# Optimization experiments

Measured on AMD Instinct MI355X. Metric: run time of the kernel, lower is better.

## Reference

```python
import jax, jax.numpy as jnp
import numpy as np

T, B, DIM, N, K = 512, 32, 1024, 256, 32  # K = checkpoint interval, divides T


def setup_inputs() -> dict:
    key = jax.random.key(0)
    k1, k2, k3, k4 = jax.random.split(key, 4)
    scale = 1.0 / np.sqrt(DIM)  # keep projections O(1) like trained weights
    return {
        "x": jax.random.normal(k1, (T, B, DIM), dtype=jnp.float32),
        "S0": jnp.zeros((B, N, N), dtype=jnp.float32),
        "W_k": jax.random.normal(k2, (N, DIM), dtype=jnp.float32) * scale,
        "W_v": jax.random.normal(k3, (N, DIM), dtype=jnp.float32) * scale,
        "W_q": jax.random.normal(k4, (N, DIM), dtype=jnp.float32) * scale,
    }


def reference(x, S0, W_k, W_v, W_q):
    # Projections (batched GEMMs), done once up-front as in the torch code.
    k_all = jnp.einsum("tbd,nd->tbn", x, W_k)
    v_all = jnp.einsum("tbd,nd->tbn", x, W_v)
    q_all = jnp.einsum("tbd,nd->tbn", x, W_q)
    k_norm = k_all / (jnp.linalg.norm(k_all, axis=-1, keepdims=True) + 1e-6)

    def step(S, kvq):
        kn, v, q = kvq  # each [B, N]
        retrieved = jnp.einsum("bij,bj->bi", S, kn)          # S @ k_norm
        S = S + (v - retrieved)[:, :, None] * kn[:, None, :]  # rank-1 delta write
        Sq = jnp.einsum("bij,bj->bi", S, q)                   # readout with updated S
        out = Sq * jax.nn.silu(Sq)
        return S, out

    def segment(S, kvq_seg):
        return jax.lax.scan(step, S, kvq_seg)

    nseg = T // K
    seg_kvq = (
        k_norm.reshape(nseg, K, B, N),
        v_all.reshape(nseg, K, B, N),
        q_all.reshape(nseg, K, B, N),
    )
    _, outs = jax.lax.scan(segment, S0, seg_kvq)  # [nseg, K, B, N]
    return outs.reshape(T, B, N)
```

## Files before the change

### kernel.cpp

```cpp
#include <hip/hip_runtime.h>
#include <hip/hip_bf16.h>
#include <math.h>

#define T_DIM 512
#define B_DIM 32
#define D_DIM 1024
#define N_DIM 256
#define M_DIM (T_DIM * B_DIM)
#define CHUNK 32
#define NCHUNK (T_DIM / CHUNK)
#define IBLK 32
#define ST (B_DIM * N_DIM)
#define BK 32

typedef _Float16 f16;
typedef _Float16 f16x8 __attribute__((ext_vector_type(8)));
typedef _Float16 f16x4 __attribute__((ext_vector_type(4)));
typedef __fp16   h16x2 __attribute__((ext_vector_type(2)));
typedef float    f32x4 __attribute__((ext_vector_type(4)));

#define LDK 264
#define LDT 40
#define LDV 36

#define GLOAD_LDS16(g, l)                                         \
  __builtin_amdgcn_global_load_lds(                               \
      (const __attribute__((address_space(1))) void*)(g),         \
      (__attribute__((address_space(3))) void*)(l), 16, 0, 0)

__device__ __forceinline__ f16x8 cvt8(const float4& a, const float4& b) {
  f16x8 h;
  h[0] = (f16)a.x; h[1] = (f16)a.y; h[2] = (f16)a.z; h[3] = (f16)a.w;
  h[4] = (f16)b.x; h[5] = (f16)b.y; h[6] = (f16)b.z; h[7] = (f16)b.w;
  return h;
}

__device__ __forceinline__ f16x8 pk8(const f32x4 a, const f32x4 b) {
  union { f16x8 v; h16x2 p[4]; } u;
  u.p[0] = __builtin_amdgcn_cvt_pkrtz(a[0], a[1]);
  u.p[1] = __builtin_amdgcn_cvt_pkrtz(a[2], a[3]);
  u.p[2] = __builtin_amdgcn_cvt_pkrtz(b[0], b[1]);
  u.p[3] = __builtin_amdgcn_cvt_pkrtz(b[2], b[3]);
  return u.v;
}

__global__ __launch_bounds__(256) void cvt_w_kernel(
    const float* __restrict__ wk, const float* __restrict__ wv,
    const float* __restrict__ wq, f16* __restrict__ out) {
  const int i = (blockIdx.x * 256 + threadIdx.x) * 8;
  const int m = blockIdx.y;
  const float* src = (m == 0) ? wk : (m == 1) ? wv : wq;
  const float4 f0 = *(const float4*)(src + i);
  const float4 f1 = *(const float4*)(src + i + 4);
  *(f16x8*)(out + (size_t)m * (N_DIM * D_DIM) + i) = cvt8(f0, f1);
}

__global__ __launch_bounds__(256, 3) void proj_gemm_mfma(
    const float* __restrict__ x, const f16* __restrict__ Wh,
    f16* __restrict__ ok, f16* __restrict__ ov, f16* __restrict__ oq) {
  __shared__ __align__(16) float Af[2][128 * BK];
  __shared__ __align__(16) f16   Bh[2][128 * BK];

  const int tid  = threadIdx.x;
  const int lane = tid & 63;
  const int w    = tid >> 6;
  const int wm   = w >> 1, wn = w & 1;
  const int lr   = lane & 15;
  const int lq   = lane >> 4;

  const int mb  = blockIdx.x * 128;
  const int mat = blockIdx.y >> 1;
  const int nb  = (blockIdx.y & 1) * 128;

  const f16* Wmat = Wh + (size_t)mat * (N_DIM * D_DIM) + (size_t)nb * D_DIM;
  f16*       C    = (mat == 0) ? ok : (mat == 1) ? ov : oq;

  const int ar  = lane >> 3;
  const int acq = (lane & 7) ^ ar;
  const int brr = lane >> 2;
  const int bco = lane & 3;

  f32x4 acc[4][4];
  #pragma unroll
  for (int i = 0; i < 4; ++i)
    #pragma unroll
    for (int j = 0; j < 4; ++j) acc[i][j] = (f32x4){0.f, 0.f, 0.f, 0.f};

  #pragma unroll
  for (int j = 0; j < 4; ++j) {
    const int r = 32 * j + 8 * w + ar;
    GLOAD_LDS16(x + (size_t)(mb + r) * D_DIM + acq * 4, &Af[0][(32 * j + 8 * w) * BK]);
  }
  #pragma unroll
  for (int j = 0; j < 2; ++j) {
    const int r = 64 * j + 16 * w + brr;
    GLOAD_LDS16(Wmat + (size_t)r * D_DIM + bco * 8, &Bh[0][(64 * j + 16 * w) * BK]);
  }
  __syncthreads();

  int cur = 0;
  for (int kt = 0; kt < D_DIM; kt += BK) {
    if (kt + BK < D_DIM) {
      #pragma unroll
      for (int j = 0; j < 4; ++j) {
        const int r = 32 * j + 8 * w + ar;
        GLOAD_LDS16(x + (size_t)(mb + r) * D_DIM + kt + BK + acq * 4,
                    &Af[cur ^ 1][(32 * j + 8 * w) * BK]);
      }
      #pragma unroll
      for (int j = 0; j < 2; ++j) {
        const int r = 64 * j + 16 * w + brr;
        GLOAD_LDS16(Wmat + (size_t)r * D_DIM + kt + BK + bco * 8,
                    &Bh[cur ^ 1][(64 * j + 16 * w) * BK]);
      }
    }
    {
      f16x8 af[4], bf[4];
      #pragma unroll
      for (int mi = 0; mi < 4; ++mi) {
        const int row = 64 * wm + 16 * mi + lr;
        const int q0  = (2 * lq)     ^ (row & 7);
        const int q1  = (2 * lq + 1) ^ (row & 7);
        const f32x4 a0 = *(const f32x4*)&Af[cur][row * BK + q0 * 4];
        const f32x4 a1 = *(const f32x4*)&Af[cur][row * BK + q1 * 4];
        af[mi] = pk8(a0, a1);
      }
      #pragma unroll
      for (int nj = 0; nj < 4; ++nj) {
        const int row = 64 * wn + 16 * nj + lr;
        bf[nj] = *(const f16x8*)&Bh[cur][row * BK + lq * 8];
      }
      #pragma unroll
      for (int mi = 0; mi < 4; ++mi)
        #pragma unroll
        for (int nj = 0; nj < 4; ++nj)
          acc[mi][nj] = __builtin_amdgcn_mfma_f32_16x16x32_f16(af[mi], bf[nj], acc[mi][nj], 0, 0, 0);
    }
    __syncthreads();
    cur ^= 1;
  }

  #pragma unroll
  for (int mi = 0; mi < 4; ++mi)
    #pragma unroll
    for (int nj = 0; nj < 4; ++nj)
      #pragma unroll
      for (int r = 0; r < 4; ++r) {
        const int rg = mb + 64 * wm + 16 * mi + 4 * lq + r;
        const int cg = nb + 64 * wn + 16 * nj + lr;
        C[(size_t)rg * N_DIM + cg] = (f16)acc[mi][nj][r];
      }
}

__global__ __launch_bounds__(256) void knorm_kernel(f16* __restrict__ k) {
  const int w    = threadIdx.x >> 6;
  const int lane = threadIdx.x & 63;
  const int row  = blockIdx.x * 4 + w;
  f16* p = k + (size_t)row * N_DIM + lane * 4;
  f16x4 h = *reinterpret_cast<const f16x4*>(p);
  const float x0 = (float)h[0], x1 = (float)h[1], x2 = (float)h[2], x3 = (float)h[3];
  float ss = x0 * x0 + x1 * x1 + x2 * x2 + x3 * x3;
  #pragma unroll
  for (int m = 1; m < 64; m <<= 1) ss += __shfl_xor(ss, m, 64);
  const float inv = 1.0f / (sqrtf(ss) + 1e-6f);
  h[0] = (f16)(x0 * inv); h[1] = (f16)(x1 * inv);
  h[2] = (f16)(x2 * inv); h[3] = (f16)(x3 * inv);
  *reinterpret_cast<f16x4*>(p) = h;
}

__global__ __launch_bounds__(256, 2) void precompute_wg(
    const f16* __restrict__ kn, const f16* __restrict__ q,
    f16* __restrict__ Wg, f16* __restrict__ Gg, f16* __restrict__ KTg) {
  __shared__ __align__(16) f16 Kh[32 * LDK];
  __shared__ __align__(16) f16 Qh[32 * LDK];
  __shared__ float Al[32 * 33];

  const int tid  = threadIdx.x;
  const int lane = tid & 63;
  const int w    = tid >> 6;
  const int lr   = lane & 15;
  const int lq   = lane >> 4;
  const int tm   = w >> 1, tn = w & 1;
  const int b    = blockIdx.x >> 4;
  const int c    = blockIdx.x & 15;
  const int t0g  = c * CHUNK;

  {
    const int t = tid >> 3, cg = tid & 7;
    const f16* ks = kn + (size_t)(t0g + t) * ST + b * N_DIM + cg * 32;
    const f16* qs = q  + (size_t)(t0g + t) * ST + b * N_DIM + cg * 32;
    #pragma unroll
    for (int m = 0; m < 4; ++m) {
      *(f16x8*)&Kh[t * LDK + cg * 32 + 8 * m] = ((const f16x8*)ks)[m];
      *(f16x8*)&Qh[t * LDK + cg * 32 + 8 * m] = ((const f16x8*)qs)[m];
    }
  }
  __syncthreads();

  {
    f16* kt_dst = KTg + ((size_t)blockIdx.x * N_DIM + tid) * CHUNK;
    #pragma unroll
    for (int t8 = 0; t8 < 4; ++t8) {
      f16x8 h;
      #pragma unroll
      for (int e = 0; e < 8; ++e) h[e] = Kh[(8 * t8 + e) * LDK + tid];
      *(f16x8*)(kt_dst + 8 * t8) = h;
    }
  }

  f32x4 Aa = {0.f, 0.f, 0.f, 0.f}, Ga = {0.f, 0.f, 0.f, 0.f};
  #pragma unroll
  for (int kk = 0; kk < 8; ++kk) {
    f16x8 ka = *(const f16x8*)&Kh[(16 * tm + lr) * LDK + 32 * kk + 8 * lq];
    f16x8 qa = *(const f16x8*)&Qh[(16 * tm + lr) * LDK + 32 * kk + 8 * lq];
    f16x8 kb = *(const f16x8*)&Kh[(16 * tn + lr) * LDK + 32 * kk + 8 * lq];
    Aa = __builtin_amdgcn_mfma_f32_16x16x32_f16(ka, kb, Aa, 0, 0, 0);
    Ga = __builtin_amdgcn_mfma_f32_16x16x32_f16(qa, kb, Ga, 0, 0, 0);
  }
  {
    const int s = 16 * tn + lr;
    f16* gdst = Gg + (size_t)blockIdx.x * 1280;
    #pragma unroll
    for (int r = 0; r < 4; ++r) {
      const int t = 16 * tm + 4 * lq + r;
      Al[t * 33 + s] = (s < t) ? Aa[r] : 0.f;
      gdst[t * LDT + s] = (f16)((s <= t) ? Ga[r] : 0.f);
    }
  }
  __syncthreads();

  if (tid < 32) {
    float wv[32];
    f16* wdst = Wg + (size_t)blockIdx.x * 1280;
    #pragma unroll
    for (int t = 0; t < 32; ++t) {
      float s0 = 0.f, s1 = 0.f, s2 = 0.f, s3 = 0.f;
      #pragma unroll
      for (int s = 0; s < 32; ++s) {
        if (s >= t) break;
        const float a = Al[t * 33 + s];
        if ((s & 3) == 0) s0 = fmaf(a, wv[s], s0);
        else if ((s & 3) == 1) s1 = fmaf(a, wv[s], s1);
        else if ((s & 3) == 2) s2 = fmaf(a, wv[s], s2);
        else s3 = fmaf(a, wv[s], s3);
      }
      wv[t] = ((t == tid) ? 1.f : 0.f) - ((s0 + s1) + (s2 + s3));
    }
    #pragma unroll
    for (int t = 0; t < 32; ++t) wdst[t * LDT + tid] = (f16)wv[t];
  }
}

__global__ __launch_bounds__(256, 1) void scan_chunked(
    const f16* __restrict__ kn, const f16* __restrict__ v,
    const f16* __restrict__ q, const float* __restrict__ S0,
    const f16* __restrict__ Wg, const f16* __restrict__ Gg,
    const f16* __restrict__ KTg, float* __restrict__ out) {
  __shared__ __align__(16) f16 Kh[32 * LDK];
  __shared__ __align__(16) f16 Qh[32 * LDK];
  __shared__ __align__(16) f16 Sh[32 * LDK];
  __shared__ __align__(16) f16 KhT[256 * LDT];
  __shared__ __align__(16) f16 Wl[32 * LDT];
  __shared__ __align__(16) f16 Gl[32 * LDT];
  __shared__ __align__(16) f16 U0T[32 * LDT];
  __shared__ __align__(16) f16 UT[32 * LDT];
  __shared__ __align__(16) float Vl[32 * LDV];

  const int tid  = threadIdx.x;
  const int lane = tid & 63;
  const int w    = tid >> 6;
  const int lr   = lane & 15;
  const int lq   = lane >> 4;
  const int tm   = w >> 1, tn = w & 1;
  const int b    = blockIdx.x & 31;
  const int i0   = (blockIdx.x >> 5) * IBLK;

  f32x4 acc[2][4];
  const float* S0b = S0 + (size_t)b * N_DIM * N_DIM + (size_t)i0 * N_DIM;
  #pragma unroll
  for (int ti = 0; ti < 2; ++ti)
    #pragma unroll
    for (int jt = 0; jt < 4; ++jt)
      #pragma unroll
      for (int r = 0; r < 4; ++r) {
        const int i = 16 * ti + 4 * lq + r;
        const int j = 64 * w + 16 * jt + lr;
        acc[ti][jt][r] = S0b[(size_t)i * N_DIM + j];
      }
  {
    const int i = tid >> 3, cg = tid & 7;
    const float* ss = S0b + (size_t)i * N_DIM + cg * 32;
    #pragma unroll
    for (int m = 0; m < 4; ++m) {
      float4 f0 = *(const float4*)(ss + 8 * m);
      float4 f1 = *(const float4*)(ss + 8 * m + 4);
      *(f16x8*)&Sh[i * LDK + cg * 32 + 8 * m] = cvt8(f0, f1);
    }
  }
  __syncthreads();

  for (int c = 0; c < NCHUNK; ++c) {
    const int t0g = c * CHUNK;
    {
      const int t = tid >> 3, cg = tid & 7;
      const f16* ks = kn + (size_t)(t0g + t) * ST + b * N_DIM + cg * 32;
      const f16* qs = q  + (size_t)(t0g + t) * ST + b * N_DIM + cg * 32;
      #pragma unroll
      for (int m = 0; m < 4; ++m) {
        *(f16x8*)&Kh[t * LDK + cg * 32 + 8 * m] = ((const f16x8*)ks)[m];
        *(f16x8*)&Qh[t * LDK + cg * 32 + 8 * m] = ((const f16x8*)qs)[m];
      }
      const f16x4 vf = *(const f16x4*)(v + (size_t)(t0g + t) * ST + b * N_DIM + i0 + cg * 4);
      *(float4*)&Vl[t * LDV + cg * 4] =
          make_float4((float)vf[0], (float)vf[1], (float)vf[2], (float)vf[3]);
    }
    {
      const f16* src = KTg + ((size_t)(b * NCHUNK + c) * N_DIM + tid) * CHUNK;
      #pragma unroll
      for (int m = 0; m < 4; ++m)
        *(f16x8*)&KhT[tid * LDT + 8 * m] = ((const f16x8*)src)[m];
    }
    if (tid < 160) {
      const f16x8* wsrc = (const f16x8*)(Wg + (size_t)(b * NCHUNK + c) * 1280);
      const f16x8* gsrc = (const f16x8*)(Gg + (size_t)(b * NCHUNK + c) * 1280);
      ((f16x8*)Wl)[tid] = wsrc[tid];
      ((f16x8*)Gl)[tid] = gsrc[tid];
    }
    __syncthreads();

    f32x4 Pacc = {0.f, 0.f, 0.f, 0.f};
    f32x4 Oq   = {0.f, 0.f, 0.f, 0.f};
    #pragma unroll
    for (int kk = 0; kk < 8; ++kk) {
      f16x8 ka = *(const f16x8*)&Kh[(16 * tm + lr) * LDK + 32 * kk + 8 * lq];
      f16x8 qa = *(const f16x8*)&Qh[(16 * tm + lr) * LDK + 32 * kk + 8 * lq];
      f16x8 sb = *(const f16x8*)&Sh[(16 * tn + lr) * LDK + 32 * kk + 8 * lq];
      Pacc = __builtin_amdgcn_mfma_f32_16x16x32_f16(ka, sb, Pacc, 0, 0, 0);
      Oq   = __builtin_amdgcn_mfma_f32_16x16x32_f16(qa, sb, Oq,   0, 0, 0);
    }
    {
      const int i = 16 * tn + lr;
      const int t0 = 16 * tm + 4 * lq;
      f16x4 u0;
      #pragma unroll
      for (int r = 0; r < 4; ++r) u0[r] = (f16)(Vl[(t0 + r) * LDV + i] - Pacc[r]);
      *(f16x4*)&U0T[i * LDT + t0] = u0;
    }
    __syncthreads();

    {
      f16x8 wa = *(const f16x8*)&Wl[(16 * tm + lr) * LDT + 8 * lq];
      f16x8 ub = *(const f16x8*)&U0T[(16 * tn + lr) * LDT + 8 * lq];
      f32x4 z = {0.f, 0.f, 0.f, 0.f};
      f32x4 Ud = __builtin_amdgcn_mfma_f32_16x16x32_f16(wa, ub, z, 0, 0, 0);
      const int i = 16 * tn + lr;
      const int t0 = 16 * tm + 4 * lq;
      f16x4 uh;
      #pragma unroll
      for (int r = 0; r < 4; ++r) uh[r] = (f16)Ud[r];
      *(f16x4*)&UT[i * LDT + t0] = uh;
    }
    __syncthreads();

    {
      f16x8 ga = *(const f16x8*)&Gl[(16 * tm + lr) * LDT + 8 * lq];
      f16x8 ub = *(const f16x8*)&UT[(16 * tn + lr) * LDT + 8 * lq];
      f32x4 O = __builtin_amdgcn_mfma_f32_16x16x32_f16(ga, ub, Oq, 0, 0, 0);
      const int i = 16 * tn + lr;
      const int tt0 = 16 * tm + 4 * lq;
      #pragma unroll
      for (int r = 0; r < 4; ++r) {
        const float sq = O[r];
        const float sig = 1.0f / (1.0f + __expf(-sq));
        out[(size_t)(t0g + tt0 + r) * ST + b * N_DIM + i0 + i] = sq * sq * sig;
      }
    }
    #pragma unroll
    for (int ti = 0; ti < 2; ++ti) {
      f16x8 ua = *(const f16x8*)&UT[(16 * ti + lr) * LDT + 8 * lq];
      #pragma unroll
      for (int jt = 0; jt < 4; ++jt) {
        f16x8 kb = *(const f16x8*)&KhT[(64 * w + 16 * jt + lr) * LDT + 8 * lq];
        acc[ti][jt] = __builtin_amdgcn_mfma_f32_16x16x32_f16(ua, kb, acc[ti][jt], 0, 0, 0);
      }
    }
    #pragma unroll
    for (int ti = 0; ti < 2; ++ti)
      #pragma unroll
      for (int jt = 0; jt < 4; ++jt)
        #pragma unroll
        for (int r = 0; r < 4; ++r)
          Sh[(16 * ti + 4 * lq + r) * LDK + 64 * w + 16 * jt + lr] = (f16)acc[ti][jt][r];
    __syncthreads();
  }
}

extern "C" void kernel_launch(void* const* d_in, const int* in_sizes, int n_in,
                              void* d_out, int out_size, void* d_ws, size_t ws_size,
                              hipStream_t stream) {
  (void)in_sizes; (void)n_in; (void)out_size; (void)ws_size;
  const float* x  = (const float*)d_in[0];
  const float* S0 = (const float*)d_in[1];
  const float* Wk = (const float*)d_in[2];
  const float* Wv = (const float*)d_in[3];
  const float* Wq = (const float*)d_in[4];
  float* outp = (float*)d_out;

  f16* kn  = (f16*)d_ws;
  f16* vv  = kn + (size_t)M_DIM * N_DIM;
  f16* qq  = vv + (size_t)M_DIM * N_DIM;
  f16* Wg  = qq + (size_t)M_DIM * N_DIM;
  f16* Gg  = Wg + (size_t)B_DIM * NCHUNK * 1280;
  f16* KTg = Gg + (size_t)B_DIM * NCHUNK * 1280;
  f16* Wh  = KTg + (size_t)B_DIM * NCHUNK * N_DIM * CHUNK;

  dim3 gw(N_DIM * D_DIM / 8 / 256, 3);
  cvt_w_kernel<<<gw, 256, 0, stream>>>(Wk, Wv, Wq, Wh);
  dim3 gg(M_DIM / 128, 6);
  proj_gemm_mfma<<<gg, 256, 0, stream>>>(x, Wh, kn, vv, qq);
  knorm_kernel<<<M_DIM / 4, 256, 0, stream>>>(kn);
  precompute_wg<<<B_DIM * NCHUNK, 256, 0, stream>>>(kn, qq, Wg, Gg, KTg);
  scan_chunked<<<B_DIM * (N_DIM / IBLK), 256, 0, stream>>>(kn, vv, qq, S0, Wg, Gg, KTg, outp);
}
```

Measured before the change: 108.6 us.

## Double scan block threads and split K-path and Q-path work across warp roles

The chunked scan kernel now runs 512 threads per block instead of 256. The first four waves compute the S·K product and the W·U correction. The other four compute the S·Q readout and the output epilogue. The state update accumulators are spread over all eight waves, so each holds half as many tiles. This is meant to raise per-block parallelism on the serial chunk loop and to overlap the two independent MFMA chains, at the cost of more threads waiting at the barriers and some waves idling in the role-specific phases.

New measurement: 102.4 us. 5.7% less time.

```diff
diff --git a/kernel.cpp b/kernel.cpp
--- a/kernel.cpp
+++ b/kernel.cpp
@@ -16,6 +16,7 @@
 typedef _Float16 f16;
 typedef _Float16 f16x8 __attribute__((ext_vector_type(8)));
 typedef _Float16 f16x4 __attribute__((ext_vector_type(4)));
+typedef _Float16 f16x2 __attribute__((ext_vector_type(2)));
 typedef __fp16   h16x2 __attribute__((ext_vector_type(2)));
 typedef float    f32x4 __attribute__((ext_vector_type(4)));
 
@@ -251,7 +252,7 @@
   }
 }
 
-__global__ __launch_bounds__(256, 1) void scan_chunked(
+__global__ __launch_bounds__(512, 1) void scan_chunked(
     const f16* __restrict__ kn, const f16* __restrict__ v,
     const f16* __restrict__ q, const float* __restrict__ S0,
     const f16* __restrict__ Wg, const f16* __restrict__ Gg,
@@ -271,30 +272,32 @@
   const int w    = tid >> 6;
   const int lr   = lane & 15;
   const int lq   = lane >> 4;
-  const int tm   = w >> 1, tn = w & 1;
+  const int role = w >> 2;
+  const int w4   = w & 3;
+  const int tm   = w4 >> 1, tn = w4 & 1;
   const int b    = blockIdx.x & 31;
   const int i0   = (blockIdx.x >> 5) * IBLK;
 
-  f32x4 acc[2][4];
+  f32x4 acc[2][2];
   const float* S0b = S0 + (size_t)b * N_DIM * N_DIM + (size_t)i0 * N_DIM;
   #pragma unroll
   for (int ti = 0; ti < 2; ++ti)
     #pragma unroll
-    for (int jt = 0; jt < 4; ++jt)
+    for (int jt = 0; jt < 2; ++jt)
       #pragma unroll
       for (int r = 0; r < 4; ++r) {
         const int i = 16 * ti + 4 * lq + r;
-        const int j = 64 * w + 16 * jt + lr;
+        const int j = 32 * w + 16 * jt + lr;
         acc[ti][jt][r] = S0b[(size_t)i * N_DIM + j];
       }
   {
-    const int i = tid >> 3, cg = tid & 7;
-    const float* ss = S0b + (size_t)i * N_DIM + cg * 32;
-    #pragma unroll
-    for (int m = 0; m < 4; ++m) {
+    const int i = tid >> 4, cg = tid & 15;
+    const float* ss = S0b + (size_t)i * N_DIM + cg * 16;
+    #pragma unroll
+    for (int m = 0; m < 2; ++m) {
       float4 f0 = *(const float4*)(ss + 8 * m);
       float4 f1 = *(const float4*)(ss + 8 * m + 4);
-      *(f16x8*)&Sh[i * LDK + cg * 32 + 8 * m] = cvt8(f0, f1);
+      *(f16x8*)&Sh[i * LDK + cg * 16 + 8 * m] = cvt8(f0, f1);
     }
   }
   __syncthreads();
@@ -302,53 +305,58 @@
   for (int c = 0; c < NCHUNK; ++c) {
     const int t0g = c * CHUNK;
     {
-      const int t = tid >> 3, cg = tid & 7;
-      const f16* ks = kn + (size_t)(t0g + t) * ST + b * N_DIM + cg * 32;
-      const f16* qs = q  + (size_t)(t0g + t) * ST + b * N_DIM + cg * 32;
-      #pragma unroll
-      for (int m = 0; m < 4; ++m) {
-        *(f16x8*)&Kh[t * LDK + cg * 32 + 8 * m] = ((const f16x8*)ks)[m];
-        *(f16x8*)&Qh[t * LDK + cg * 32 + 8 * m] = ((const f16x8*)qs)[m];
-      }
-      const f16x4 vf = *(const f16x4*)(v + (size_t)(t0g + t) * ST + b * N_DIM + i0 + cg * 4);
-      *(float4*)&Vl[t * LDV + cg * 4] =
-          make_float4((float)vf[0], (float)vf[1], (float)vf[2], (float)vf[3]);
+      const int t = tid >> 4, cg = tid & 15;
+      const f16* ks = kn + (size_t)(t0g + t) * ST + b * N_DIM + cg * 16;
+      const f16* qs = q  + (size_t)(t0g + t) * ST + b * N_DIM + cg * 16;
+      #pragma unroll
+      for (int m = 0; m < 2; ++m) {
+        *(f16x8*)&Kh[t * LDK + cg * 16 + 8 * m] = ((const f16x8*)ks)[m];
+        *(f16x8*)&Qh[t * LDK + cg * 16 + 8 * m] = ((const f16x8*)qs)[m];
+      }
+      const int c2 = (tid & 15) * 2;
+      const f16x2 vf = *(const f16x2*)(v + (size_t)(t0g + t) * ST + b * N_DIM + i0 + c2);
+      *(float2*)&Vl[t * LDV + c2] = make_float2((float)vf[0], (float)vf[1]);
     }
     {
-      const f16* src = KTg + ((size_t)(b * NCHUNK + c) * N_DIM + tid) * CHUNK;
-      #pragma unroll
-      for (int m = 0; m < 4; ++m)
-        *(f16x8*)&KhT[tid * LDT + 8 * m] = ((const f16x8*)src)[m];
+      const int row = tid >> 1, m0 = (tid & 1) * 2;
+      const f16* src = KTg + ((size_t)(b * NCHUNK + c) * N_DIM + row) * CHUNK;
+      #pragma unroll
+      for (int m = 0; m < 2; ++m)
+        *(f16x8*)&KhT[row * LDT + 8 * (m0 + m)] = ((const f16x8*)src)[m0 + m];
     }
     if (tid < 160) {
-      const f16x8* wsrc = (const f16x8*)(Wg + (size_t)(b * NCHUNK + c) * 1280);
-      const f16x8* gsrc = (const f16x8*)(Gg + (size_t)(b * NCHUNK + c) * 1280);
-      ((f16x8*)Wl)[tid] = wsrc[tid];
-      ((f16x8*)Gl)[tid] = gsrc[tid];
+      ((f16x8*)Wl)[tid] = ((const f16x8*)(Wg + (size_t)(b * NCHUNK + c) * 1280))[tid];
+    } else if (tid < 320) {
+      ((f16x8*)Gl)[tid - 160] = ((const f16x8*)(Gg + (size_t)(b * NCHUNK + c) * 1280))[tid - 160];
     }
     __syncthreads();
 
-    f32x4 Pacc = {0.f, 0.f, 0.f, 0.f};
-    f32x4 Oq   = {0.f, 0.f, 0.f, 0.f};
-    #pragma unroll
-    for (int kk = 0; kk < 8; ++kk) {
-      f16x8 ka = *(const f16x8*)&Kh[(16 * tm + lr) * LDK + 32 * kk + 8 * lq];
-      f16x8 qa = *(const f16x8*)&Qh[(16 * tm + lr) * LDK + 32 * kk + 8 * lq];
-      f16x8 sb = *(const f16x8*)&Sh[(16 * tn + lr) * LDK + 32 * kk + 8 * lq];
-      Pacc = __builtin_amdgcn_mfma_f32_16x16x32_f16(ka, sb, Pacc, 0, 0, 0);
-      Oq   = __builtin_amdgcn_mfma_f32_16x16x32_f16(qa, sb, Oq,   0, 0, 0);
-    }
-    {
+    f32x4 Oq = {0.f, 0.f, 0.f, 0.f};
+    if (role == 0) {
+      f32x4 Pacc = {0.f, 0.f, 0.f, 0.f};
+      #pragma unroll
+      for (int kk = 0; kk < 8; ++kk) {
+        f16x8 ka = *(const f16x8*)&Kh[(16 * tm + lr) * LDK + 32 * kk + 8 * lq];
+        f16x8 sb = *(const f16x8*)&Sh[(16 * tn + lr) * LDK + 32 * kk + 8 * lq];
+        Pacc = __builtin_amdgcn_mfma_f32_16x16x32_f16(ka, sb, Pacc, 0, 0, 0);
+      }
       const int i = 16 * tn + lr;
       const int t0 = 16 * tm + 4 * lq;
       f16x4 u0;
       #pragma unroll
       for (int r = 0; r < 4; ++r) u0[r] = (f16)(Vl[(t0 + r) * LDV + i] - Pacc[r]);
       *(f16x4*)&U0T[i * LDT + t0] = u0;
+    } else {
+      #pragma unroll
+      for (int kk = 0; kk < 8; ++kk) {
+        f16x8 qa = *(const f16x8*)&Qh[(16 * tm + lr) * LDK + 32 * kk + 8 * lq];
+        f16x8 sb = *(const f16x8*)&Sh[(16 * tn + lr) * LDK + 32 * kk + 8 * lq];
+        Oq = __builtin_amdgcn_mfma_f32_16x16x32_f16(qa, sb, Oq, 0, 0, 0);
+      }
     }
     __syncthreads();
 
-    {
+    if (role == 0) {
       f16x8 wa = *(const f16x8*)&Wl[(16 * tm + lr) * LDT + 8 * lq];
       f16x8 ub = *(const f16x8*)&U0T[(16 * tn + lr) * LDT + 8 * lq];
       f32x4 z = {0.f, 0.f, 0.f, 0.f};
@@ -362,7 +370,7 @@
     }
     __syncthreads();
 
-    {
+    if (role == 1) {
       f16x8 ga = *(const f16x8*)&Gl[(16 * tm + lr) * LDT + 8 * lq];
       f16x8 ub = *(const f16x8*)&UT[(16 * tn + lr) * LDT + 8 * lq];
       f32x4 O = __builtin_amdgcn_mfma_f32_16x16x32_f16(ga, ub, Oq, 0, 0, 0);
@@ -379,18 +387,18 @@
     for (int ti = 0; ti < 2; ++ti) {
       f16x8 ua = *(const f16x8*)&UT[(16 * ti + lr) * LDT + 8 * lq];
       #pragma unroll
-      for (int jt = 0; jt < 4; ++jt) {
-        f16x8 kb = *(const f16x8*)&KhT[(64 * w + 16 * jt + lr) * LDT + 8 * lq];
+      for (int jt = 0; jt < 2; ++jt) {
+        f16x8 kb = *(const f16x8*)&KhT[(32 * w + 16 * jt + lr) * LDT + 8 * lq];
         acc[ti][jt] = __builtin_amdgcn_mfma_f32_16x16x32_f16(ua, kb, acc[ti][jt], 0, 0, 0);
       }
     }
     #pragma unroll
     for (int ti = 0; ti < 2; ++ti)
       #pragma unroll
-      for (int jt = 0; jt < 4; ++jt)
+      for (int jt = 0; jt < 2; ++jt)
         #pragma unroll
         for (int r = 0; r < 4; ++r)
-          Sh[(16 * ti + 4 * lq + r) * LDK + 64 * w + 16 * jt + lr] = (f16)acc[ti][jt][r];
+          Sh[(16 * ti + 4 * lq + r) * LDK + 32 * w + 16 * jt + lr] = (f16)acc[ti][jt][r];
     __syncthreads();
   }
 }
@@ -420,5 +428,5 @@
   proj_gemm_mfma<<<gg, 256, 0, stream>>>(x, Wh, kn, vv, qq);
   knorm_kernel<<<M_DIM / 4, 256, 0, stream>>>(kn);
   precompute_wg<<<B_DIM * NCHUNK, 256, 0, stream>>>(kn, qq, Wg, Gg, KTg);
-  scan_chunked<<<B_DIM * (N_DIM / IBLK), 256, 0, stream>>>(kn, vv, qq, S0, Wg, Gg, KTg, outp);
-}
+  scan_chunked<<<B_DIM * (N_DIM / IBLK), 512, 0, stream>>>(kn, vv, qq, S0, Wg, Gg, KTg, outp);
+}
```
